# Optimization experiments

Measured on AMD Instinct MI355X. Metric: run time of the kernel, lower is better.

Reference implementation:

```python
import jax, jax.numpy as jnp
import numpy as np

B, N, DIM, H, DH = 8, 1024, 1024, 16, 64

def setup_inputs() -> dict:
    key = jax.random.key(0)
    ks = jax.random.split(key, 6)
    return {
        'x': jax.random.normal(ks[0], (B, N, DIM), dtype=jnp.float32),
        'freqs': jax.random.normal(ks[1], (1, N, DH), dtype=jnp.float32),
        'bias': jax.random.normal(ks[2], (1, N, DH), dtype=jnp.float32),
        'ln_gamma': jnp.ones((DIM,), jnp.float32),
        'ln_beta': jnp.zeros((DIM,), jnp.float32),
        'w_qk': jax.random.normal(ks[3], (DIM, 2 * H * DH), dtype=jnp.float32) * (DIM ** -0.5),
        'w_v': jax.random.normal(ks[4], (DIM, H * DH), dtype=jnp.float32) * (DIM ** -0.5),
        'w_out': jax.random.normal(ks[5], (H * DH, DIM), dtype=jnp.float32) * ((H * DH) ** -0.5),
        'b_out': jnp.zeros((DIM,), jnp.float32),
    }

def _apply_polar(t, freqs):
    # t: [b,h,n,d]; freqs: [1,n,d] broadcast over b,h. Output doubles last dim.
    t = jax.nn.softplus(t)
    return jnp.concatenate((t * jnp.cos(freqs), t * jnp.sin(freqs)), axis=-1)

def reference(x, freqs, bias, ln_gamma, ln_beta, w_qk, w_v, w_out, b_out):
    eps = 1e-5
    mu = jnp.mean(x, axis=-1, keepdims=True)
    var = jnp.var(x, axis=-1, keepdims=True)
    xn = (x - mu) * jax.lax.rsqrt(var + eps) * ln_gamma + ln_beta
    qk = jnp.einsum('bnd,de->bne', xn, w_qk)
    q, k = jnp.split(qk, 2, axis=-1)
    v = jnp.einsum('bnd,de->bne', xn, w_v)
    split_heads = lambda t: t.reshape(B, N, H, DH).transpose(0, 2, 1, 3)
    q, k, v = split_heads(q), split_heads(k), split_heads(v)
    q = _apply_polar(q, freqs)          # [b,h,n,2*DH]
    k = _apply_polar(k, freqs + bias)   # [b,h,n,2*DH]
    scale = DH ** -0.5
    dots = jnp.einsum('bhnd,bhmd->bhnm', q, k) * scale
    attn = jax.nn.softmax(dots, axis=-1)
    out = jnp.einsum('bhnm,bhmd->bhnd', attn, v)
    out = out.transpose(0, 2, 1, 3).reshape(B, N, H * DH)
    return jnp.einsum('bne,ed->bnd', out, w_out) + b_out
```

## Files before the change

kernel.cpp:

```cpp
#include <hip/hip_runtime.h>
#include <cmath>

using f16   = _Float16;
using f16x2 = __attribute__((ext_vector_type(2))) _Float16;
using f16x4 = __attribute__((ext_vector_type(4))) _Float16;
using f16x8 = __attribute__((ext_vector_type(8))) _Float16;
using f32x4 = __attribute__((ext_vector_type(4))) float;

#define DEV __device__ __forceinline__

constexpr int Bb  = 8;
constexpr int Nn  = 1024;
constexpr int DIM = 1024;
constexpr int Hh  = 16;
constexpr int DH  = 64;
constexpr int EQKV = 3072;

DEV void async16(const f16* g, f16* l) {
  __builtin_amdgcn_global_load_lds(
      (const __attribute__((address_space(1))) void*)g,
      (__attribute__((address_space(3))) void*)l, 16, 0, 0);
}

DEV float softplusf(float x) {
  return fmaxf(x, 0.f) + __logf(1.f + __expf(-fabsf(x)));
}

__global__ __launch_bounds__(256) void transpose_cvt3(const float* __restrict__ s0,
                                                      const float* __restrict__ s1,
                                                      const float* __restrict__ s2,
                                                      f16* __restrict__ d0,
                                                      f16* __restrict__ d2) {
  __shared__ float tile[32][33];
  const float* src; f16* dst; int cols;
  int bz = blockIdx.z;
  if (bz == 0)      { src = s0; dst = d0;                        cols = 2048; }
  else if (bz == 1) { src = s1; dst = d0 + (size_t)2048 * 1024;  cols = 1024; }
  else              { src = s2; dst = d2;                        cols = 1024; }
  int c0 = blockIdx.x * 32, r0 = blockIdx.y * 32;
  if (c0 >= cols) return;
  int t = threadIdx.x, tx = t & 31, ty = t >> 5;
#pragma unroll
  for (int j = 0; j < 32; j += 8)
    tile[ty + j][tx] = src[(size_t)(r0 + ty + j) * cols + c0 + tx];
  __syncthreads();
#pragma unroll
  for (int j = 0; j < 32; j += 8)
    dst[(size_t)(c0 + ty + j) * 1024 + r0 + tx] = (f16)tile[tx][ty + j];
}

__global__ __launch_bounds__(256) void trig_prep(const float* __restrict__ freqs,
                                                 const float* __restrict__ fbias,
                                                 float4* __restrict__ trig) {
  int i = blockIdx.x * 256 + threadIdx.x;
  float f = freqs[i], fb = fbias[i];
  float cq, sq, ck, sk;
  __sincosf(f, &sq, &cq);
  __sincosf(f + fb, &sk, &ck);
  trig[i] = make_float4(cq, sq, ck, sk);
}

__global__ __launch_bounds__(256) void ln_kernel(const float* __restrict__ x,
                                                 const float* __restrict__ gamma,
                                                 const float* __restrict__ beta,
                                                 f16* __restrict__ xn) {
  int row = blockIdx.x;
  int t = threadIdx.x;
  const float4* xr = (const float4*)(x + (size_t)row * DIM);
  float4 v = xr[t];
  float s  = v.x + v.y + v.z + v.w;
  float s2 = v.x * v.x + v.y * v.y + v.z * v.z + v.w * v.w;
#pragma unroll
  for (int off = 32; off; off >>= 1) {
    s  += __shfl_xor(s,  off, 64);
    s2 += __shfl_xor(s2, off, 64);
  }
  __shared__ float red[8];
  int wv = t >> 6, lane = t & 63;
  if (lane == 0) { red[wv] = s; red[4 + wv] = s2; }
  __syncthreads();
  s  = red[0] + red[1] + red[2] + red[3];
  s2 = red[4] + red[5] + red[6] + red[7];
  float mu  = s * (1.f / DIM);
  float var = s2 * (1.f / DIM) - mu * mu;
  float rs  = rsqrtf(var + 1e-5f);
  float4 g = ((const float4*)gamma)[t];
  float4 bb = ((const float4*)beta)[t];
  f16x4 o;
  o[0] = (f16)((v.x - mu) * rs * g.x + bb.x);
  o[1] = (f16)((v.y - mu) * rs * g.y + bb.y);
  o[2] = (f16)((v.z - mu) * rs * g.z + bb.z);
  o[3] = (f16)((v.w - mu) * rs * g.w + bb.w);
  ((f16x4*)(xn + (size_t)row * DIM))[t] = o;
}

template <bool FP32OUT>
__global__ __launch_bounds__(256) void gemm_bt(const f16* __restrict__ A,
                                               const f16* __restrict__ Bt,
                                               void* __restrict__ Cv,
                                               const float* __restrict__ bias,
                                               int M, int K, int E) {
  __shared__ f16 lA[128 * 32];
  __shared__ f16 lB[128 * 32];
  int tid  = threadIdx.x;
  int lane = tid & 63;
  int wv   = __builtin_amdgcn_readfirstlane(tid >> 6);
  int nbe  = E >> 7;
  int bm = blockIdx.x / nbe, be = blockIdx.x % nbe;
  size_t m0 = (size_t)bm * 128, e0 = (size_t)be * 128;
  int wm = (wv & 1) * 64, we = (wv >> 1) * 64;
  int lm = lane & 15, q = lane >> 4;

  f32x4 acc[4][4] = {};

  int row_s[2], cg_s[2];
#pragma unroll
  for (int r = 0; r < 2; ++r) {
    int s = r * 256 + tid;
    row_s[r] = s >> 2;
    cg_s[r]  = (s & 3) ^ ((row_s[r] >> 1) & 3);
  }
  const f16* pa[4];
  const f16* pb[4];
#pragma unroll
  for (int i = 0; i < 4; ++i) {
    int ra = wm + i * 16 + lm;
    pa[i] = lA + ra * 32 + (q ^ ((ra >> 1) & 3)) * 8;
    int rb = we + i * 16 + lm;
    pb[i] = lB + rb * 32 + (q ^ ((rb >> 1) & 3)) * 8;
  }

  for (int k0 = 0; k0 < K; k0 += 32) {
#pragma unroll
    for (int r = 0; r < 2; ++r) {
      const f16* ga = A  + (m0 + row_s[r]) * K + k0 + cg_s[r] * 8;
      const f16* gb = Bt + (e0 + row_s[r]) * K + k0 + cg_s[r] * 8;
      async16(ga, lA + (r * 256 + wv * 64) * 8);
      async16(gb, lB + (r * 256 + wv * 64) * 8);
    }
    __syncthreads();
    f16x8 af[4], bf[4];
#pragma unroll
    for (int i = 0; i < 4; ++i) {
      af[i] = *(const f16x8*)pa[i];
      bf[i] = *(const f16x8*)pb[i];
    }
#pragma unroll
    for (int i = 0; i < 4; ++i)
#pragma unroll
      for (int j = 0; j < 4; ++j)
        acc[i][j] = __builtin_amdgcn_mfma_f32_16x16x32_f16(af[i], bf[j], acc[i][j], 0, 0, 0);
    __syncthreads();
  }

#pragma unroll
  for (int i = 0; i < 4; ++i) {
    size_t mbase = m0 + wm + i * 16 + q * 4;
#pragma unroll
    for (int j = 0; j < 4; ++j) {
      size_t e = e0 + we + j * 16 + lm;
#pragma unroll
      for (int g = 0; g < 4; ++g) {
        float val = acc[i][j][g];
        if (FP32OUT)
          ((float*)Cv)[(mbase + g) * (size_t)E + e] = val + bias[e];
        else
          ((f16*)Cv)[(mbase + g) * (size_t)E + e] = (f16)val;
      }
    }
  }
}

__global__ __launch_bounds__(256, 3) void gemm_qkv(const f16* __restrict__ A,
                                                   const f16* __restrict__ Bt,
                                                   f16* __restrict__ Qp,
                                                   f16* __restrict__ Kp,
                                                   f16* __restrict__ Vn,
                                                   const float4* __restrict__ trig,
                                                   int M, int K) {
  __shared__ f16 lA[128 * 32];
  __shared__ f16 lB[128 * 32];
  int tid  = threadIdx.x;
  int lane = tid & 63;
  int wv   = __builtin_amdgcn_readfirstlane(tid >> 6);
  const int nbe = 24;
  const int cpx = gridDim.x >> 3;
  int bid = blockIdx.x;
  int swz = (bid & 7) * cpx + (bid >> 3);
  int bm = swz / nbe, be = swz % nbe;
  size_t m0 = (size_t)bm * 128, e0 = (size_t)be * 128;
  int wm = (wv & 1) * 64, we = (wv >> 1) * 64;
  int lm = lane & 15, q = lane >> 4;

  f32x4 acc[4][4] = {};

  int row_s[2], cg_s[2];
#pragma unroll
  for (int r = 0; r < 2; ++r) {
    int s = r * 256 + tid;
    row_s[r] = s >> 2;
    cg_s[r]  = (s & 3) ^ ((row_s[r] >> 1) & 3);
  }
  const f16* pa[4];
  const f16* pb[4];
#pragma unroll
  for (int i = 0; i < 4; ++i) {
    int ra = wm + i * 16 + lm;
    pa[i] = lA + ra * 32 + (q ^ ((ra >> 1) & 3)) * 8;
    int rb = we + i * 16 + lm;
    pb[i] = lB + rb * 32 + (q ^ ((rb >> 1) & 3)) * 8;
  }

  for (int k0 = 0; k0 < K; k0 += 32) {
#pragma unroll
    for (int r = 0; r < 2; ++r) {
      const f16* ga = A  + (m0 + row_s[r]) * K + k0 + cg_s[r] * 8;
      const f16* gb = Bt + (e0 + row_s[r]) * K + k0 + cg_s[r] * 8;
      async16(ga, lA + (r * 256 + wv * 64) * 8);
      async16(gb, lB + (r * 256 + wv * 64) * 8);
    }
    __syncthreads();
    f16x8 af[4], bf[4];
#pragma unroll
    for (int i = 0; i < 4; ++i) {
      af[i] = *(const f16x8*)pa[i];
      bf[i] = *(const f16x8*)pb[i];
    }
#pragma unroll
    for (int i = 0; i < 4; ++i)
#pragma unroll
      for (int j = 0; j < 4; ++j)
        acc[i][j] = __builtin_amdgcn_mfma_f32_16x16x32_f16(af[i], bf[j], acc[i][j], 0, 0, 0);
    __syncthreads();
  }

  const int sec = be >> 3;
  if (sec < 2) {
    f16* dst = (sec == 0) ? Qp : Kp;
    const float scl = (sec == 0) ? 0.125f : 1.0f;
#pragma unroll
    for (int i = 0; i < 4; ++i) {
      size_t mbase = m0 + wm + i * 16 + q * 4;
#pragma unroll
      for (int j = 0; j < 4; ++j) {
        int hd = (int)((e0 + we + j * 16 + lm) & 1023);
        int h = hd >> 6, d = hd & 63;
#pragma unroll
        for (int g = 0; g < 4; ++g) {
          size_t tok = mbase + g;
          int n = (int)(tok & 1023);
          size_t bh = (tok >> 10) * 16 + h;
          float sp = softplusf(acc[i][j][g]) * scl;
          float4 T = trig[n * 64 + d];
          float c = (sec == 0) ? T.x : T.z;
          float s = (sec == 0) ? T.y : T.w;
          f16x2 o = { (f16)(sp * c), (f16)(sp * s) };
          *(f16x2*)(dst + (bh * (size_t)Nn + n) * 128 + 2 * d) = o;
        }
      }
    }
  } else {
#pragma unroll
    for (int i = 0; i < 4; ++i) {
      size_t mbase = m0 + wm + i * 16 + q * 4;
#pragma unroll
      for (int j = 0; j < 4; ++j) {
        int hd = (int)((e0 + we + j * 16 + lm) & 1023);
#pragma unroll
        for (int g = 0; g < 4; ++g)
          Vn[(mbase + g) * 1024 + hd] = (f16)acc[i][j][g];
      }
    }
  }
}

__global__ __launch_bounds__(256) void vtrans_kernel(const f16* __restrict__ Vn,
                                                     f16* __restrict__ Vt) {
  __shared__ f16 vt[64 * 66];
  int tid = threadIdx.x;
  int bx = blockIdx.x;
  int nt = bx & 15, bh = bx >> 4;
  int b = bh >> 4, h = bh & 15;
  size_t tok0 = (size_t)b * Nn + nt * 64;
  int n0 = nt * 64;
#pragma unroll
  for (int i = 0; i < 8; ++i) {
    int e2 = tid + i * 256;
    int nl = e2 >> 5, dp = (e2 & 31) * 2;
    f16x2 v2 = *(const f16x2*)(Vn + (tok0 + nl) * 1024 + h * 64 + dp);
    vt[dp * 66 + nl]       = v2[0];
    vt[(dp + 1) * 66 + nl] = v2[1];
  }
  __syncthreads();
#pragma unroll
  for (int i = 0; i < 16; ++i) {
    int e = tid + i * 256;
    int d = e >> 6, nl = e & 63;
    Vt[((size_t)bh * 64 + d) * Nn + n0 + nl] = vt[d * 66 + nl];
  }
}

constexpr int VK0 = 0;
constexpr int VK1 = 8192;
constexpr int VV0 = 16384;
constexpr int VV1 = 21504;
constexpr int VEND = 26624;

__global__ __launch_bounds__(256, 3) void attn_kernel(const f16* __restrict__ Qp,
                                                      const f16* __restrict__ Kp,
                                                      const f16* __restrict__ Vt,
                                                      f16* __restrict__ attout) {
  __shared__ f16 smem[VEND];

  int tid = threadIdx.x, lane = tid & 63;
  int wv = __builtin_amdgcn_readfirstlane(tid >> 6);
  int lm = lane & 15, q = lane >> 4;
  int bx = blockIdx.x;
  int bh = (bx & 7) | ((bx >> 6) << 3);
  int qt = (bx >> 3) & 7;
  const f16* Kbase = Kp + (size_t)bh * Nn * 128;
  const f16* Vbase = Vt + (size_t)bh * 64 * Nn;

  {
    int idx = tid * 4;
    f16 val = (idx < 64) ? (f16)1.0f : (f16)0.0f;
    f16x4 v4 = {val, val, val, val};
    *(f16x4*)(smem + VV0 + 64 * 64 + idx) = v4;
    *(f16x4*)(smem + VV1 + 64 * 64 + idx) = v4;
  }

#pragma unroll
  for (int i = 0; i < 4; ++i) {
    int s = i * 256 + tid;
    int r = s >> 4, c = s & 15;
    int g = c ^ (r & 15);
    async16(Kbase + (size_t)r * 128 + g * 8, smem + VK0 + (i * 256 + wv * 64) * 8);
  }
#pragma unroll
  for (int i = 0; i < 2; ++i) {
    int s = i * 256 + tid;
    int r = s >> 3, c = s & 7;
    int g = c ^ (r & 7);
    async16(Vbase + (size_t)r * Nn + g * 8, smem + VV0 + (i * 256 + wv * 64) * 8);
  }

  f16x8 qf[2][4];
  {
    const f16* Qb = Qp + ((size_t)bh * Nn + qt * 128 + wv * 32) * 128;
#pragma unroll
    for (int grp = 0; grp < 2; ++grp)
#pragma unroll
      for (int ks = 0; ks < 4; ++ks)
        qf[grp][ks] = *(const f16x8*)(Qb + (size_t)(grp * 16 + lm) * 128 + ks * 32 + q * 8);
  }

  f32x4 O[2][5] = {};
  float mrow[2] = {-INFINITY, -INFINITY};

  for (int kt = 0; kt < 16; ++kt) {
    __syncthreads();

    if (kt < 15) {
      f16* nK = smem + ((kt & 1) ? VK0 : VK1);
      f16* nV = smem + ((kt & 1) ? VV0 : VV1);
#pragma unroll
      for (int i = 0; i < 4; ++i) {
        int s = i * 256 + tid;
        int r = s >> 4, c = s & 15;
        int g = c ^ (r & 15);
        async16(Kbase + (size_t)((kt + 1) * 64 + r) * 128 + g * 8, nK + (i * 256 + wv * 64) * 8);
      }
#pragma unroll
      for (int i = 0; i < 2; ++i) {
        int s = i * 256 + tid;
        int r = s >> 3, c = s & 7;
        int g = c ^ (r & 7);
        async16(Vbase + (size_t)r * Nn + (kt + 1) * 64 + g * 8, nV + (i * 256 + wv * 64) * 8);
      }
    }
    const f16* sK = smem + ((kt & 1) ? VK1 : VK0);
    const f16* sV = smem + ((kt & 1) ? VV1 : VV0);

    f32x4 S[2][4] = {};
#pragma unroll
    for (int nt = 0; nt < 4; ++nt) {
      f16x8 kf[4];
#pragma unroll
      for (int ks = 0; ks < 4; ++ks)
        kf[ks] = *(const f16x8*)(sK + (nt * 16 + lm) * 128 + (((ks * 4 + q) ^ lm) * 8));
#pragma unroll
      for (int ks = 0; ks < 4; ++ks) {
        S[0][nt] = __builtin_amdgcn_mfma_f32_16x16x32_f16(kf[ks], qf[0][ks], S[0][nt], 0, 0, 0);
        S[1][nt] = __builtin_amdgcn_mfma_f32_16x16x32_f16(kf[ks], qf[1][ks], S[1][nt], 0, 0, 0);
      }
    }

    f16x4 pf[2][4];
#pragma unroll
    for (int grp = 0; grp < 2; ++grp) {
      float mx = -INFINITY;
#pragma unroll
      for (int nt = 0; nt < 4; ++nt)
#pragma unroll
        for (int g = 0; g < 4; ++g) mx = fmaxf(mx, S[grp][nt][g]);
      mx = fmaxf(mx, __shfl_xor(mx, 16, 64));
      mx = fmaxf(mx, __shfl_xor(mx, 32, 64));
      float mn = fmaxf(mrow[grp], mx);
      float alpha = __expf(mrow[grp] - mn);
      mrow[grp] = mn;
#pragma unroll
      for (int nt = 0; nt < 4; ++nt)
#pragma unroll
        for (int g = 0; g < 4; ++g)
          pf[grp][nt][g] = (f16)__expf(S[grp][nt][g] - mn);
#pragma unroll
      for (int nto = 0; nto < 5; ++nto)
#pragma unroll
        for (int g = 0; g < 4; ++g) O[grp][nto][g] *= alpha;
    }

#pragma unroll
    for (int nto = 0; nto < 5; ++nto) {
      int r = nto * 16 + lm;
#pragma unroll
      for (int nt = 0; nt < 4; ++nt) {
        int c16 = (nt * 2 + (q >> 1)) ^ (r & 7);
        f16x4 vf = *(const f16x4*)(sV + r * 64 + c16 * 8 + (q & 1) * 4);
        O[0][nto] = __builtin_amdgcn_mfma_f32_16x16x16f16(vf, pf[0][nt], O[0][nto], 0, 0, 0);
        O[1][nto] = __builtin_amdgcn_mfma_f32_16x16x16f16(vf, pf[1][nt], O[1][nto], 0, 0, 0);
      }
    }
  }

  int b = bh >> 4, h = bh & 15;
#pragma unroll
  for (int grp = 0; grp < 2; ++grp) {
    float l = __shfl(O[grp][4][0], lm, 64);
    float inv = 1.f / l;
    size_t token = (size_t)b * Nn + qt * 128 + wv * 32 + grp * 16 + lm;
#pragma unroll
    for (int nto = 0; nto < 4; ++nto) {
      f16x4 o4;
#pragma unroll
      for (int g = 0; g < 4; ++g) o4[g] = (f16)(O[grp][nto][g] * inv);
      *(f16x4*)(attout + token * (size_t)(Hh * DH) + h * 64 + nto * 16 + q * 4) = o4;
    }
  }
}

extern "C" void kernel_launch(void* const* d_in, const int* in_sizes, int n_in,
                              void* d_out, int out_size, void* d_ws, size_t ws_size,
                              hipStream_t stream) {
  const float* x     = (const float*)d_in[0];
  const float* freqs = (const float*)d_in[1];
  const float* fbias = (const float*)d_in[2];
  const float* gamma = (const float*)d_in[3];
  const float* beta  = (const float*)d_in[4];
  const float* w_qk  = (const float*)d_in[5];
  const float* w_v   = (const float*)d_in[6];
  const float* w_out = (const float*)d_in[7];
  const float* b_out = (const float*)d_in[8];
  float* out = (float*)d_out;

  const size_t T = (size_t)Bb * Nn;
  f16* WqkvT = (f16*)d_ws;
  f16* WoutT = WqkvT + (size_t)EQKV * DIM;
  float4* trig = (float4*)(WoutT + (size_t)DIM * DIM);
  f16* Xn    = (f16*)(trig + (size_t)Nn * DH);
  f16* Vn    = Xn + T * DIM;
  f16* AttO  = Vn + T * DIM;
  f16* Qp    = AttO + T * DIM;
  f16* Kp    = Qp + (size_t)128 * Nn * 128;
  f16* Vt    = Kp + (size_t)128 * Nn * 128;

  transpose_cvt3<<<dim3(64, 32, 3), 256, 0, stream>>>(w_qk, w_v, w_out, WqkvT, WoutT);

  trig_prep<<<(Nn * DH) / 256, 256, 0, stream>>>(freqs, fbias, trig);

  ln_kernel<<<(int)T, 256, 0, stream>>>(x, gamma, beta, Xn);

  gemm_qkv<<<(int)(T / 128) * (EQKV / 128), 256, 0, stream>>>(
      Xn, WqkvT, Qp, Kp, Vn, trig, (int)T, DIM);

  vtrans_kernel<<<Bb * Hh * (Nn / 64), 256, 0, stream>>>(Vn, Vt);

  attn_kernel<<<Bb * Hh * (Nn / 128), 256, 0, stream>>>(Qp, Kp, Vt, AttO);

  gemm_bt<true><<<(int)(T / 128) * (DIM / 128), 256, 0, stream>>>(
      AttO, WoutT, (void*)out, b_out, (int)T, DIM, DIM);
}
```

Baseline: 287.5 us.

## Fuse V transpose into QKV GEMM epilogue and split trig tables

The separate vtrans kernel goes away. The V section of the QKV GEMM now stages its output tile in a larger shared buffer and writes the transposed V layout directly with 16-byte stores. This removes a full round trip of V through global memory plus one kernel launch. The trig table is also split into separate Q and K float2 arrays, so each epilogue loads only the cosine/sine pair it needs. In exchange, shared memory per block grows from 16 KB to about 34 KB, which may limit the requested three blocks per CU.

```diff
diff --git a/kernel.cpp b/kernel.cpp
--- a/kernel.cpp
+++ b/kernel.cpp
@@ -51,13 +51,15 @@
 
 __global__ __launch_bounds__(256) void trig_prep(const float* __restrict__ freqs,
                                                  const float* __restrict__ fbias,
-                                                 float4* __restrict__ trig) {
+                                                 float2* __restrict__ trigQ,
+                                                 float2* __restrict__ trigK) {
   int i = blockIdx.x * 256 + threadIdx.x;
   float f = freqs[i], fb = fbias[i];
   float cq, sq, ck, sk;
   __sincosf(f, &sq, &cq);
   __sincosf(f + fb, &sk, &ck);
-  trig[i] = make_float4(cq, sq, ck, sk);
+  trigQ[i] = make_float2(cq, sq);
+  trigK[i] = make_float2(ck, sk);
 }
 
 __global__ __launch_bounds__(256) void ln_kernel(const float* __restrict__ x,
@@ -175,11 +177,13 @@
                                                    const f16* __restrict__ Bt,
                                                    f16* __restrict__ Qp,
                                                    f16* __restrict__ Kp,
-                                                   f16* __restrict__ Vn,
-                                                   const float4* __restrict__ trig,
+                                                   f16* __restrict__ Vt,
+                                                   const float2* __restrict__ trigQ,
+                                                   const float2* __restrict__ trigK,
                                                    int M, int K) {
-  __shared__ f16 lA[128 * 32];
-  __shared__ f16 lB[128 * 32];
+  __shared__ f16 smem[17408];
+  f16* lA = smem;
+  f16* lB = smem + 4096;
   int tid  = threadIdx.x;
   int lane = tid & 63;
   int wv   = __builtin_amdgcn_readfirstlane(tid >> 6);
@@ -237,6 +241,7 @@
   const int sec = be >> 3;
   if (sec < 2) {
     f16* dst = (sec == 0) ? Qp : Kp;
+    const float2* trig = (sec == 0) ? trigQ : trigK;
     const float scl = (sec == 0) ? 0.125f : 1.0f;
 #pragma unroll
     for (int i = 0; i < 4; ++i) {
@@ -251,52 +256,36 @@
           int n = (int)(tok & 1023);
           size_t bh = (tok >> 10) * 16 + h;
           float sp = softplusf(acc[i][j][g]) * scl;
-          float4 T = trig[n * 64 + d];
-          float c = (sec == 0) ? T.x : T.z;
-          float s = (sec == 0) ? T.y : T.w;
-          f16x2 o = { (f16)(sp * c), (f16)(sp * s) };
+          float2 T = trig[n * 64 + d];
+          f16x2 o = { (f16)(sp * T.x), (f16)(sp * T.y) };
           *(f16x2*)(dst + (bh * (size_t)Nn + n) * 128 + 2 * d) = o;
         }
       }
     }
   } else {
+    __syncthreads();
 #pragma unroll
     for (int i = 0; i < 4; ++i) {
-      size_t mbase = m0 + wm + i * 16 + q * 4;
+      int nl = wm + i * 16 + q * 4;
 #pragma unroll
       for (int j = 0; j < 4; ++j) {
-        int hd = (int)((e0 + we + j * 16 + lm) & 1023);
+        int ds = we + j * 16 + lm;
 #pragma unroll
         for (int g = 0; g < 4; ++g)
-          Vn[(mbase + g) * 1024 + hd] = (f16)acc[i][j][g];
-      }
-    }
-  }
-}
-
-__global__ __launch_bounds__(256) void vtrans_kernel(const f16* __restrict__ Vn,
-                                                     f16* __restrict__ Vt) {
-  __shared__ f16 vt[64 * 66];
-  int tid = threadIdx.x;
-  int bx = blockIdx.x;
-  int nt = bx & 15, bh = bx >> 4;
-  int b = bh >> 4, h = bh & 15;
-  size_t tok0 = (size_t)b * Nn + nt * 64;
-  int n0 = nt * 64;
-#pragma unroll
-  for (int i = 0; i < 8; ++i) {
-    int e2 = tid + i * 256;
-    int nl = e2 >> 5, dp = (e2 & 31) * 2;
-    f16x2 v2 = *(const f16x2*)(Vn + (tok0 + nl) * 1024 + h * 64 + dp);
-    vt[dp * 66 + nl]       = v2[0];
-    vt[(dp + 1) * 66 + nl] = v2[1];
-  }
-  __syncthreads();
-#pragma unroll
-  for (int i = 0; i < 16; ++i) {
-    int e = tid + i * 256;
-    int d = e >> 6, nl = e & 63;
-    Vt[((size_t)bh * 64 + d) * Nn + n0 + nl] = vt[d * 66 + nl];
+          smem[ds * 136 + nl + g] = (f16)acc[i][j][g];
+      }
+    }
+    __syncthreads();
+    const int nbase = (int)(m0 & 1023);
+    const size_t bh0 = (m0 >> 10) * 16 + ((e0 & 1023) >> 6);
+#pragma unroll
+    for (int k = 0; k < 8; ++k) {
+      int c = k * 256 + tid;
+      int row = c >> 4, ch = c & 15;
+      int h = row >> 6, d = row & 63;
+      f16x8 v8 = *(const f16x8*)(smem + row * 136 + ch * 8);
+      *(f16x8*)(Vt + ((bh0 + h) * (size_t)64 + d) * Nn + nbase + ch * 8) = v8;
+    }
   }
 }
 
@@ -465,24 +454,22 @@
   const size_t T = (size_t)Bb * Nn;
   f16* WqkvT = (f16*)d_ws;
   f16* WoutT = WqkvT + (size_t)EQKV * DIM;
-  float4* trig = (float4*)(WoutT + (size_t)DIM * DIM);
-  f16* Xn    = (f16*)(trig + (size_t)Nn * DH);
-  f16* Vn    = Xn + T * DIM;
-  f16* AttO  = Vn + T * DIM;
+  float2* trigQ = (float2*)(WoutT + (size_t)DIM * DIM);
+  float2* trigK = trigQ + (size_t)Nn * DH;
+  f16* Xn    = (f16*)(trigK + (size_t)Nn * DH);
+  f16* AttO  = Xn + T * DIM;
   f16* Qp    = AttO + T * DIM;
   f16* Kp    = Qp + (size_t)128 * Nn * 128;
   f16* Vt    = Kp + (size_t)128 * Nn * 128;
 
   transpose_cvt3<<<dim3(64, 32, 3), 256, 0, stream>>>(w_qk, w_v, w_out, WqkvT, WoutT);
 
-  trig_prep<<<(Nn * DH) / 256, 256, 0, stream>>>(freqs, fbias, trig);
+  trig_prep<<<(Nn * DH) / 256, 256, 0, stream>>>(freqs, fbias, trigQ, trigK);
 
   ln_kernel<<<(int)T, 256, 0, stream>>>(x, gamma, beta, Xn);
 
   gemm_qkv<<<(int)(T / 128) * (EQKV / 128), 256, 0, stream>>>(
-      Xn, WqkvT, Qp, Kp, Vn, trig, (int)T, DIM);
-
-  vtrans_kernel<<<Bb * Hh * (Nn / 64), 256, 0, stream>>>(Vn, Vt);
+      Xn, WqkvT, Qp, Kp, Vt, trigQ, trigK, (int)T, DIM);
 
   attn_kernel<<<Bb * Hh * (Nn / 128), 256, 0, stream>>>(Qp, Kp, Vt, AttO);
 
```

New measurement: 277.5 us. 3.5% less time.
